# Kernel optimization log

Measured on AMD Instinct MI355X. Metric: run time of the kernel, lower is better.

## Reference

```python
import jax, jax.numpy as jnp
import numpy as np

N_NOTE = 14  # undefined global in original; must equal output_size for one-hot feedback


def setup_inputs() -> dict:
    key = jax.random.key(0)
    ks = jax.random.split(key, 9)
    B, T, H, O = 256, 512, 2048, 14
    s_i = 1.0 / np.sqrt(14)
    s_h = 1.0 / np.sqrt(H)
    return {
        "encoder_outputs": jax.random.normal(ks[0], (B, 1, H), jnp.float32),
        "encoder_hidden": jax.random.normal(ks[1], (1, B, H), jnp.float32),
        "target_tensor": jax.random.uniform(ks[2], (B, T, O), jnp.float32),
        "W_ih": jax.random.normal(ks[3], (3 * H, 14), jnp.float32) * s_i,
        "W_hh": jax.random.normal(ks[4], (3 * H, H), jnp.float32) * s_h,
        "b_ih": jax.random.normal(ks[5], (3 * H,), jnp.float32) * s_h,
        "b_hh": jax.random.normal(ks[6], (3 * H,), jnp.float32) * s_h,
        "W_out": jax.random.normal(ks[7], (O, H), jnp.float32) * s_h,
        "b_out": jax.random.normal(ks[8], (O,), jnp.float32) * s_h,
    }


def _decode(encoder_hidden, target_tensor, W_ih, W_hh, b_ih, b_hh, W_out, b_out):
    B, T, O = target_tensor.shape
    H = W_hh.shape[1]

    def step(carry, _):
        h, x = carry  # h: [B,H], x: [B,14]
        xr = jax.nn.relu(x)
        gi = xr @ W_ih.T + b_ih            # [B,3H]
        gh = h @ W_hh.T + b_hh             # [B,3H]
        r = jax.nn.sigmoid(gi[:, :H] + gh[:, :H])
        z = jax.nn.sigmoid(gi[:, H:2 * H] + gh[:, H:2 * H])
        n = jnp.tanh(gi[:, 2 * H:] + r * gh[:, 2 * H:])
        h_new = (1.0 - z) * n + z * h
        logits = h_new @ W_out.T + b_out   # [B,O]
        # feedback: one-hot of argmax; the Python `break` in the original zeros
        # every batch element at-or-after the first hit of n_note-1
        topi = jnp.argmax(logits, axis=-1)                     # [B]
        hit = (topi == N_NOTE - 1).astype(jnp.int32)
        alive = (jnp.cumsum(hit) == 0).astype(logits.dtype)    # inclusive cumsum
        x_next = jax.nn.one_hot(topi, O, dtype=logits.dtype) * alive[:, None]
        return (h_new, x_next), logits

    h0 = encoder_hidden[0]          # [B,H]
    x0 = target_tensor[:, 0]        # [B,14] first-step input
    (h_final, _), logits = jax.lax.scan(step, (h0, x0), None, length=T)
    logits = jnp.transpose(logits, (1, 0, 2))  # [B,T,O]
    log_probs = jax.nn.log_softmax(logits, axis=-1)
    return log_probs, h_final[None]  # ([B,T,O], [1,B,H])


def reference(encoder_outputs, encoder_hidden, target_tensor, W_ih, W_hh, b_ih, b_hh, W_out, b_out):
    # encoder_outputs is accepted but unused, matching the original forward
    return _decode(encoder_hidden, target_tensor, W_ih, W_hh, b_ih, b_hh, W_out, b_out)
```

## Files before the change

kernel.cpp:

```cpp
#include <hip/hip_runtime.h>
#include <math.h>

typedef float f4 __attribute__((ext_vector_type(4)));
typedef _Float16 f16x8 __attribute__((ext_vector_type(8)));
typedef int i4 __attribute__((ext_vector_type(4)));

#define Hdim 2048
#define Bdim 256
#define Tdim 512
#define Odim 14
#define G3   6144


__global__ void prep_gtable(const float* __restrict__ b_ih,
                            const float* __restrict__ W_ih,
                            float* __restrict__ Gt) {
    int idx = blockIdx.x * 256 + threadIdx.x;
    if (idx >= 15 * G3) return;
    int c = idx / G3, row = idx % G3;
    float v = b_ih[row];
    if (c < Odim) v += W_ih[row * Odim + c];
    Gt[idx] = v;
}

__global__ void prep_gi0(const float* __restrict__ b_ih,
                         const float* __restrict__ W_ih,
                         const float* __restrict__ target,
                         float* __restrict__ gi0) {
    int idx = blockIdx.x * 256 + threadIdx.x;
    int b = idx / G3, row = idx % G3;
    const float* x0 = target + (size_t)b * (Tdim * Odim);
    float s = b_ih[row];
    #pragma unroll
    for (int c = 0; c < Odim; ++c)
        s = fmaf(fmaxf(x0[c], 0.f), W_ih[row * Odim + c], s);
    gi0[idx] = s;
}

__global__ void prep_Bpack(const float* __restrict__ W,
                           _Float16* __restrict__ Bh, _Float16* __restrict__ Bl) {
    int idx = blockIdx.x * 256 + threadIdx.x;
    int n = idx >> 8, kc = idx & 255;
    const float* src = W + (size_t)n * Hdim + kc * 8;
    int kb = kc >> 2, q = kc & 3;
    int lane = (n & 15) + 16 * q;
    int nt = n >> 4;
    f16x8 vh, vl;
    #pragma unroll
    for (int j = 0; j < 8; ++j) {
        float w = src[j];
        _Float16 h = (_Float16)w;
        vh[j] = h;
        vl[j] = (_Float16)(w - (float)h);
    }
    size_t off = (((size_t)nt * 64 + kb) * 64 + lane) * 8;
    *(f16x8*)(Bh + off) = vh;
    *(f16x8*)(Bl + off) = vl;
}

__global__ void prep_A0(const float* __restrict__ h0,
                        _Float16* __restrict__ Ah, _Float16* __restrict__ Al) {
    int idx = blockIdx.x * 256 + threadIdx.x;
    int m = idx >> 8, kc = idx & 255;
    const float* src = h0 + (size_t)m * Hdim + kc * 8;
    int kb = kc >> 2, q = kc & 3;
    int lane = (m & 15) + 16 * q;
    int mt = m >> 4;
    f16x8 vh, vl;
    #pragma unroll
    for (int j = 0; j < 8; ++j) {
        float w = src[j];
        _Float16 h = (_Float16)w;
        vh[j] = h;
        vl[j] = (_Float16)(w - (float)h);
    }
    size_t off = (((size_t)mt * 64 + kb) * 64 + lane) * 8;
    *(f16x8*)(Ah + off) = vh;
    *(f16x8*)(Al + off) = vl;
}

__global__ __launch_bounds__(512, 1)
void gemm_step(const _Float16* __restrict__ Ah, const _Float16* __restrict__ Al,
               const _Float16* __restrict__ Bh, const _Float16* __restrict__ Bl,
               float* __restrict__ Cpart) {
    __shared__ __align__(16) _Float16 sB[2][24576];

    const int tid = threadIdx.x;
    const int wave = tid >> 6, lane = tid & 63;
    const int nt0 = blockIdx.x * 6;
    const int kb0 = blockIdx.y * 16;

    f4 acc[2][6];
    #pragma unroll
    for (int mf = 0; mf < 2; ++mf)
        #pragma unroll
        for (int nf = 0; nf < 6; ++nf) acc[mf][nf] = (f4)0.f;

    i4 rh[3], rl[3];

    #pragma unroll
    for (int i = 0; i < 3; ++i) {
        int e = i * 512 + tid, blk = e >> 6, l = e & 63;
        int ntl = blk >> 2, kbl = blk & 3;
        size_t off = (((size_t)(nt0 + ntl) * 64) + kb0 + kbl) * 512 + l * 8;
        rh[i] = *(const i4*)(Bh + off);
        rl[i] = *(const i4*)(Bl + off);
    }
    #pragma unroll
    for (int i = 0; i < 3; ++i) {
        ((i4*)sB[0])[i * 512 + tid] = rh[i];
        ((i4*)sB[0])[1536 + i * 512 + tid] = rl[i];
    }
    __syncthreads();

    for (int c = 0; c < 4; ++c) {
        const int buf = c & 1;
        if (c < 3) {
            #pragma unroll
            for (int i = 0; i < 3; ++i) {
                int e = i * 512 + tid, blk = e >> 6, l = e & 63;
                int ntl = blk >> 2, kbl = blk & 3;
                size_t off = (((size_t)(nt0 + ntl) * 64) + kb0 + (c + 1) * 4 + kbl) * 512 + l * 8;
                rh[i] = *(const i4*)(Bh + off);
                rl[i] = *(const i4*)(Bl + off);
            }
        }
        #pragma unroll
        for (int kbl = 0; kbl < 4; ++kbl) {
            const int kb = kb0 + c * 4 + kbl;
            f16x8 a_h[2], a_l[2], b_h[6], b_l[6];
            #pragma unroll
            for (int mf = 0; mf < 2; ++mf) {
                size_t off = (((size_t)(wave * 2 + mf) * 64 + kb) * 64 + lane) * 8;
                a_h[mf] = *(const f16x8*)(Ah + off);
                a_l[mf] = *(const f16x8*)(Al + off);
            }
            #pragma unroll
            for (int nf = 0; nf < 6; ++nf) {
                int base = (nf * 4 + kbl) * 512 + lane * 8;
                b_h[nf] = *(const f16x8*)(&sB[buf][base]);
                b_l[nf] = *(const f16x8*)(&sB[buf][12288 + base]);
            }
            #pragma unroll
            for (int mf = 0; mf < 2; ++mf)
                #pragma unroll
                for (int nf = 0; nf < 6; ++nf) {
                    acc[mf][nf] = __builtin_amdgcn_mfma_f32_16x16x32_f16(
                        a_h[mf], b_h[nf], acc[mf][nf], 0, 0, 0);
                    acc[mf][nf] = __builtin_amdgcn_mfma_f32_16x16x32_f16(
                        a_h[mf], b_l[nf], acc[mf][nf], 0, 0, 0);
                    acc[mf][nf] = __builtin_amdgcn_mfma_f32_16x16x32_f16(
                        a_l[mf], b_h[nf], acc[mf][nf], 0, 0, 0);
                }
        }
        if (c < 3) {
            __syncthreads();
            #pragma unroll
            for (int i = 0; i < 3; ++i) {
                ((i4*)sB[buf ^ 1])[i * 512 + tid] = rh[i];
                ((i4*)sB[buf ^ 1])[1536 + i * 512 + tid] = rl[i];
            }
            __syncthreads();
        }
    }

    const size_t base = (size_t)blockIdx.y * 256 * G3;
    #pragma unroll
    for (int mf = 0; mf < 2; ++mf) {
        int mrow = wave * 32 + mf * 16 + (lane >> 4) * 4;
        #pragma unroll
        for (int nf = 0; nf < 6; ++nf) {
            int n = (nt0 + nf) * 16 + (lane & 15);
            #pragma unroll
            for (int q = 0; q < 4; ++q)
                Cpart[base + (size_t)(mrow + q) * G3 + n] = acc[mf][nf][q];
        }
    }
}

__global__ __launch_bounds__(256)
void fused_out(const float* __restrict__ hprev, float* __restrict__ hnew,
               const float* __restrict__ Cpart, const float* __restrict__ Gt,
               const float* __restrict__ gi0, const float* __restrict__ b_hh,
               const float* __restrict__ W_out, const float* __restrict__ b_out,
               _Float16* __restrict__ Ah, _Float16* __restrict__ Al,
               const int* __restrict__ topi_in, int* __restrict__ topi_out,
               float* __restrict__ lp, float* __restrict__ hfin, int t) {
    const int b = blockIdx.x;
    const int tid = threadIdx.x;
    __shared__ __align__(16) float sh[Hdim];
    __shared__ float sl[16];
    __shared__ int s_sel;
    __shared__ unsigned long long s_m[4];

    if (t > 0) {
        int tp = topi_in[tid];
        unsigned long long m = __ballot(tp == (Odim - 1));
        if ((tid & 63) == 0) s_m[tid >> 6] = m;
        __syncthreads();
        if (tid == 0) {
            int bw = b >> 6, bl = b & 63;
            unsigned long long le =
                s_m[bw] & ((bl == 63) ? ~0ULL : ((1ULL << (bl + 1)) - 1ULL));
            bool dead = (le != 0ULL);
            for (int w = 0; w < bw; ++w) dead = dead || (s_m[w] != 0ULL);
            s_sel = dead ? Odim : topi_in[b];
        }
        __syncthreads();
    }
    const float* gp = (t == 0) ? (gi0 + (size_t)b * G3)
                               : (Gt + (size_t)s_sel * G3);

    const int j0 = tid * 8;
    float hn[8];
    {
        float gsum[3][8];
        #pragma unroll
        for (int g = 0; g < 3; ++g) {
            f4 s0 = *(const f4*)(b_hh + g * Hdim + j0);
            f4 s1 = *(const f4*)(b_hh + g * Hdim + j0 + 4);
            #pragma unroll
            for (int c = 0; c < 4; ++c) { gsum[g][c] = s0[c]; gsum[g][4 + c] = s1[c]; }
            #pragma unroll
            for (int ks = 0; ks < 4; ++ks) {
                const float* cp = Cpart + ((size_t)ks * Bdim + b) * G3 + g * Hdim + j0;
                f4 p0 = *(const f4*)cp;
                f4 p1 = *(const f4*)(cp + 4);
                #pragma unroll
                for (int c = 0; c < 4; ++c) { gsum[g][c] += p0[c]; gsum[g][4 + c] += p1[c]; }
            }
        }
        f4 hp0 = *(const f4*)(hprev + (size_t)b * Hdim + j0);
        f4 hp1 = *(const f4*)(hprev + (size_t)b * Hdim + j0 + 4);
        f4 gr0 = *(const f4*)(gp + j0),            gr1 = *(const f4*)(gp + j0 + 4);
        f4 gz0 = *(const f4*)(gp + Hdim + j0),     gz1 = *(const f4*)(gp + Hdim + j0 + 4);
        f4 gn0 = *(const f4*)(gp + 2 * Hdim + j0), gn1 = *(const f4*)(gp + 2 * Hdim + j0 + 4);
        #pragma unroll
        for (int c = 0; c < 8; ++c) {
            float gi_r = (c < 4) ? gr0[c] : gr1[c - 4];
            float gi_z = (c < 4) ? gz0[c] : gz1[c - 4];
            float gi_n = (c < 4) ? gn0[c] : gn1[c - 4];
            float hp   = (c < 4) ? hp0[c] : hp1[c - 4];
            float rr = 1.f / (1.f + expf(-(gi_r + gsum[0][c])));
            float zz = 1.f / (1.f + expf(-(gi_z + gsum[1][c])));
            float nn = tanhf(fmaf(rr, gsum[2][c], gi_n));
            hn[c] = (1.f - zz) * nn + zz * hp;
        }
    }
    f4 o0, o1;
    #pragma unroll
    for (int c = 0; c < 4; ++c) { o0[c] = hn[c]; o1[c] = hn[4 + c]; }
    *(f4*)(hnew + (size_t)b * Hdim + j0) = o0;
    *(f4*)(hnew + (size_t)b * Hdim + j0 + 4) = o1;
    {
        f16x8 vh, vl;
        #pragma unroll
        for (int c = 0; c < 8; ++c) {
            _Float16 hh = (_Float16)hn[c];
            vh[c] = hh;
            vl[c] = (_Float16)(hn[c] - (float)hh);
        }
        int kb = tid >> 2, q = tid & 3;
        int lane = (b & 15) + 16 * q, mt = b >> 4;
        size_t off = (((size_t)mt * 64 + kb) * 64 + lane) * 8;
        *(f16x8*)(Ah + off) = vh;
        *(f16x8*)(Al + off) = vl;
    }
    *(f4*)(sh + j0) = o0;
    *(f4*)(sh + j0 + 4) = o1;
    __syncthreads();

    const int w = tid >> 6, l = tid & 63;
    for (int o = w; o < Odim; o += 4) {
        const float* wo = W_out + (size_t)o * Hdim;
        float s = 0.f;
        #pragma unroll
        for (int i = 0; i < 32; ++i)
            s = fmaf(sh[l + 64 * i], wo[l + 64 * i], s);
        #pragma unroll
        for (int off = 32; off >= 1; off >>= 1)
            s += __shfl_down(s, off);
        if (l == 0) sl[o] = s + b_out[o];
    }
    __syncthreads();
    if (tid == 0) {
        float m = sl[0]; int bi = 0;
        #pragma unroll
        for (int o = 1; o < Odim; ++o)
            if (sl[o] > m) { m = sl[o]; bi = o; }
        float ssum = 0.f;
        #pragma unroll
        for (int o = 0; o < Odim; ++o) ssum += expf(sl[o] - m);
        topi_out[b] = bi;
        sl[14] = m + logf(ssum);
    }
    __syncthreads();
    if (tid < Odim)
        lp[(size_t)b * (Tdim * Odim) + (size_t)t * Odim + tid] = sl[tid] - sl[14];
    if (hfin) {
        *(f4*)(hfin + (size_t)b * Hdim + j0) = o0;
        *(f4*)(hfin + (size_t)b * Hdim + j0 + 4) = o1;
    }
}

extern "C" void kernel_launch(void* const* d_in, const int* in_sizes, int n_in,
                              void* d_out, int out_size, void* d_ws, size_t ws_size,
                              hipStream_t stream) {
    const float* enc_hidden = (const float*)d_in[1];
    const float* target     = (const float*)d_in[2];
    const float* W_ih       = (const float*)d_in[3];
    const float* W_hh       = (const float*)d_in[4];
    const float* b_ih       = (const float*)d_in[5];
    const float* b_hh       = (const float*)d_in[6];
    const float* W_out      = (const float*)d_in[7];
    const float* b_out      = (const float*)d_in[8];

    float* out  = (float*)d_out;
    float* lp   = out;
    float* hfin = out + (size_t)Bdim * Tdim * Odim;

    float* ws    = (float*)d_ws;
    float* hb0   = ws;
    float* hb1   = hb0 + 524288;
    float* Gt    = hb1 + 524288;
    float* gi0   = Gt + 15 * G3;
    float* Cpart = gi0 + (size_t)Bdim * G3;
    _Float16* Ah = (_Float16*)(Cpart + 4 * (size_t)Bdim * G3);
    _Float16* Al = Ah + (size_t)Bdim * Hdim;
    _Float16* Bh = Al + (size_t)Bdim * Hdim;
    _Float16* Bl = Bh + (size_t)G3 * Hdim;
    int* topibuf = (int*)(Bl + (size_t)G3 * Hdim);

    prep_gtable<<<(15 * G3 + 255) / 256, 256, 0, stream>>>(b_ih, W_ih, Gt);
    prep_gi0<<<(Bdim * G3) / 256, 256, 0, stream>>>(b_ih, W_ih, target, gi0);
    prep_Bpack<<<(G3 * 256) / 256, 256, 0, stream>>>(W_hh, Bh, Bl);
    prep_A0<<<(Bdim * 256) / 256, 256, 0, stream>>>(enc_hidden, Ah, Al);

    for (int t = 0; t < Tdim; ++t) {
        float* hnew = (t & 1) ? hb1 : hb0;
        const float* hprev = (t == 0) ? enc_hidden : ((t & 1) ? hb0 : hb1);
        int* tin  = topibuf + ((t + 1) & 1) * 256;
        int* tout = topibuf + (t & 1) * 256;
        gemm_step<<<dim3(64, 4), 512, 0, stream>>>(Ah, Al, Bh, Bl, Cpart);
        fused_out<<<256, 256, 0, stream>>>(hprev, hnew, Cpart, Gt, gi0, b_hh,
                                           W_out, b_out, Ah, Al, tin, tout, lp,
                                           (t == Tdim - 1) ? hfin : nullptr, t);
    }
}
```

Baseline: 19.93 ms.

## Retile recurrent GEMM to 3 N-tiles with 2-way K split, widen fused_out

```diff
diff --git a/kernel.cpp b/kernel.cpp
--- a/kernel.cpp
+++ b/kernel.cpp
@@ -3,6 +3,7 @@
 
 typedef float f4 __attribute__((ext_vector_type(4)));
 typedef _Float16 f16x8 __attribute__((ext_vector_type(8)));
+typedef _Float16 f16x4 __attribute__((ext_vector_type(4)));
 typedef int i4 __attribute__((ext_vector_type(4)));
 
 #define Hdim 2048
@@ -79,7 +80,7 @@
     *(f16x8*)(Al + off) = vl;
 }
 
-__global__ __launch_bounds__(512, 1)
+__global__ __launch_bounds__(512, 2)
 void gemm_step(const _Float16* __restrict__ Ah, const _Float16* __restrict__ Al,
                const _Float16* __restrict__ Bh, const _Float16* __restrict__ Bl,
                float* __restrict__ Cpart) {
@@ -87,21 +88,21 @@
 
     const int tid = threadIdx.x;
     const int wave = tid >> 6, lane = tid & 63;
-    const int nt0 = blockIdx.x * 6;
-    const int kb0 = blockIdx.y * 16;
-
-    f4 acc[2][6];
+    const int nt0 = blockIdx.x * 3;
+    const int kb0 = blockIdx.y * 32;
+
+    f4 acc[2][3];
     #pragma unroll
     for (int mf = 0; mf < 2; ++mf)
         #pragma unroll
-        for (int nf = 0; nf < 6; ++nf) acc[mf][nf] = (f4)0.f;
+        for (int nf = 0; nf < 3; ++nf) acc[mf][nf] = (f4)0.f;
 
     i4 rh[3], rl[3];
 
     #pragma unroll
     for (int i = 0; i < 3; ++i) {
         int e = i * 512 + tid, blk = e >> 6, l = e & 63;
-        int ntl = blk >> 2, kbl = blk & 3;
+        int ntl = blk >> 3, kbl = blk & 7;
         size_t off = (((size_t)(nt0 + ntl) * 64) + kb0 + kbl) * 512 + l * 8;
         rh[i] = *(const i4*)(Bh + off);
         rl[i] = *(const i4*)(Bl + off);
@@ -119,16 +120,16 @@
             #pragma unroll
             for (int i = 0; i < 3; ++i) {
                 int e = i * 512 + tid, blk = e >> 6, l = e & 63;
-                int ntl = blk >> 2, kbl = blk & 3;
-                size_t off = (((size_t)(nt0 + ntl) * 64) + kb0 + (c + 1) * 4 + kbl) * 512 + l * 8;
+                int ntl = blk >> 3, kbl = blk & 7;
+                size_t off = (((size_t)(nt0 + ntl) * 64) + kb0 + (c + 1) * 8 + kbl) * 512 + l * 8;
                 rh[i] = *(const i4*)(Bh + off);
                 rl[i] = *(const i4*)(Bl + off);
             }
         }
         #pragma unroll
-        for (int kbl = 0; kbl < 4; ++kbl) {
-            const int kb = kb0 + c * 4 + kbl;
-            f16x8 a_h[2], a_l[2], b_h[6], b_l[6];
+        for (int kbl = 0; kbl < 8; ++kbl) {
+            const int kb = kb0 + c * 8 + kbl;
+            f16x8 a_h[2], a_l[2], b_h[3], b_l[3];
             #pragma unroll
             for (int mf = 0; mf < 2; ++mf) {
                 size_t off = (((size_t)(wave * 2 + mf) * 64 + kb) * 64 + lane) * 8;
@@ -136,15 +137,15 @@
                 a_l[mf] = *(const f16x8*)(Al + off);
             }
             #pragma unroll
-            for (int nf = 0; nf < 6; ++nf) {
-                int base = (nf * 4 + kbl) * 512 + lane * 8;
+            for (int nf = 0; nf < 3; ++nf) {
+                int base = ((nf * 8 + kbl) * 64 + lane) * 8;
                 b_h[nf] = *(const f16x8*)(&sB[buf][base]);
                 b_l[nf] = *(const f16x8*)(&sB[buf][12288 + base]);
             }
             #pragma unroll
             for (int mf = 0; mf < 2; ++mf)
                 #pragma unroll
-                for (int nf = 0; nf < 6; ++nf) {
+                for (int nf = 0; nf < 3; ++nf) {
                     acc[mf][nf] = __builtin_amdgcn_mfma_f32_16x16x32_f16(
                         a_h[mf], b_h[nf], acc[mf][nf], 0, 0, 0);
                     acc[mf][nf] = __builtin_amdgcn_mfma_f32_16x16x32_f16(
@@ -164,12 +165,12 @@
         }
     }
 
-    const size_t base = (size_t)blockIdx.y * 256 * G3;
+    const size_t base = (size_t)blockIdx.y * Bdim * G3;
     #pragma unroll
     for (int mf = 0; mf < 2; ++mf) {
         int mrow = wave * 32 + mf * 16 + (lane >> 4) * 4;
         #pragma unroll
-        for (int nf = 0; nf < 6; ++nf) {
+        for (int nf = 0; nf < 3; ++nf) {
             int n = (nt0 + nf) * 16 + (lane & 15);
             #pragma unroll
             for (int q = 0; q < 4; ++q)
@@ -178,7 +179,7 @@
     }
 }
 
-__global__ __launch_bounds__(256)
+__global__ __launch_bounds__(512)
 void fused_out(const float* __restrict__ hprev, float* __restrict__ hnew,
                const float* __restrict__ Cpart, const float* __restrict__ Gt,
                const float* __restrict__ gi0, const float* __restrict__ b_hh,
@@ -194,9 +195,11 @@
     __shared__ unsigned long long s_m[4];
 
     if (t > 0) {
-        int tp = topi_in[tid];
-        unsigned long long m = __ballot(tp == (Odim - 1));
-        if ((tid & 63) == 0) s_m[tid >> 6] = m;
+        if (tid < 256) {
+            int tp = topi_in[tid];
+            unsigned long long m = __ballot(tp == (Odim - 1));
+            if ((tid & 63) == 0) s_m[tid >> 6] = m;
+        }
         __syncthreads();
         if (tid == 0) {
             int bw = b >> 6, bl = b & 63;
@@ -211,67 +214,54 @@
     const float* gp = (t == 0) ? (gi0 + (size_t)b * G3)
                                : (Gt + (size_t)s_sel * G3);
 
-    const int j0 = tid * 8;
-    float hn[8];
+    const int j0 = tid * 4;
+    float hn[4];
     {
-        float gsum[3][8];
+        float gsum[3][4];
         #pragma unroll
         for (int g = 0; g < 3; ++g) {
-            f4 s0 = *(const f4*)(b_hh + g * Hdim + j0);
-            f4 s1 = *(const f4*)(b_hh + g * Hdim + j0 + 4);
-            #pragma unroll
-            for (int c = 0; c < 4; ++c) { gsum[g][c] = s0[c]; gsum[g][4 + c] = s1[c]; }
-            #pragma unroll
-            for (int ks = 0; ks < 4; ++ks) {
-                const float* cp = Cpart + ((size_t)ks * Bdim + b) * G3 + g * Hdim + j0;
-                f4 p0 = *(const f4*)cp;
-                f4 p1 = *(const f4*)(cp + 4);
-                #pragma unroll
-                for (int c = 0; c < 4; ++c) { gsum[g][c] += p0[c]; gsum[g][4 + c] += p1[c]; }
-            }
-        }
-        f4 hp0 = *(const f4*)(hprev + (size_t)b * Hdim + j0);
-        f4 hp1 = *(const f4*)(hprev + (size_t)b * Hdim + j0 + 4);
-        f4 gr0 = *(const f4*)(gp + j0),            gr1 = *(const f4*)(gp + j0 + 4);
-        f4 gz0 = *(const f4*)(gp + Hdim + j0),     gz1 = *(const f4*)(gp + Hdim + j0 + 4);
-        f4 gn0 = *(const f4*)(gp + 2 * Hdim + j0), gn1 = *(const f4*)(gp + 2 * Hdim + j0 + 4);
-        #pragma unroll
-        for (int c = 0; c < 8; ++c) {
-            float gi_r = (c < 4) ? gr0[c] : gr1[c - 4];
-            float gi_z = (c < 4) ? gz0[c] : gz1[c - 4];
-            float gi_n = (c < 4) ? gn0[c] : gn1[c - 4];
-            float hp   = (c < 4) ? hp0[c] : hp1[c - 4];
-            float rr = 1.f / (1.f + expf(-(gi_r + gsum[0][c])));
-            float zz = 1.f / (1.f + expf(-(gi_z + gsum[1][c])));
-            float nn = tanhf(fmaf(rr, gsum[2][c], gi_n));
-            hn[c] = (1.f - zz) * nn + zz * hp;
-        }
-    }
-    f4 o0, o1;
-    #pragma unroll
-    for (int c = 0; c < 4; ++c) { o0[c] = hn[c]; o1[c] = hn[4 + c]; }
+            f4 s = *(const f4*)(b_hh + g * Hdim + j0);
+            #pragma unroll
+            for (int ks = 0; ks < 2; ++ks)
+                s += *(const f4*)(Cpart + ((size_t)ks * Bdim + b) * G3 + g * Hdim + j0);
+            #pragma unroll
+            for (int c = 0; c < 4; ++c) gsum[g][c] = s[c];
+        }
+        f4 hp = *(const f4*)(hprev + (size_t)b * Hdim + j0);
+        f4 gr = *(const f4*)(gp + j0);
+        f4 gz = *(const f4*)(gp + Hdim + j0);
+        f4 gn = *(const f4*)(gp + 2 * Hdim + j0);
+        #pragma unroll
+        for (int c = 0; c < 4; ++c) {
+            float rr = 1.f / (1.f + expf(-(gr[c] + gsum[0][c])));
+            float zz = 1.f / (1.f + expf(-(gz[c] + gsum[1][c])));
+            float nn = tanhf(fmaf(rr, gsum[2][c], gn[c]));
+            hn[c] = (1.f - zz) * nn + zz * hp[c];
+        }
+    }
+    f4 o0;
+    #pragma unroll
+    for (int c = 0; c < 4; ++c) o0[c] = hn[c];
     *(f4*)(hnew + (size_t)b * Hdim + j0) = o0;
-    *(f4*)(hnew + (size_t)b * Hdim + j0 + 4) = o1;
     {
-        f16x8 vh, vl;
-        #pragma unroll
-        for (int c = 0; c < 8; ++c) {
+        f16x4 vh, vl;
+        #pragma unroll
+        for (int c = 0; c < 4; ++c) {
             _Float16 hh = (_Float16)hn[c];
             vh[c] = hh;
             vl[c] = (_Float16)(hn[c] - (float)hh);
         }
-        int kb = tid >> 2, q = tid & 3;
+        int kb = j0 >> 5, q = (j0 >> 3) & 3, e0 = j0 & 7;
         int lane = (b & 15) + 16 * q, mt = b >> 4;
-        size_t off = (((size_t)mt * 64 + kb) * 64 + lane) * 8;
-        *(f16x8*)(Ah + off) = vh;
-        *(f16x8*)(Al + off) = vl;
+        size_t off = (((size_t)mt * 64 + kb) * 64 + lane) * 8 + e0;
+        *(f16x4*)(Ah + off) = vh;
+        *(f16x4*)(Al + off) = vl;
     }
     *(f4*)(sh + j0) = o0;
-    *(f4*)(sh + j0 + 4) = o1;
     __syncthreads();
 
     const int w = tid >> 6, l = tid & 63;
-    for (int o = w; o < Odim; o += 4) {
+    for (int o = w; o < Odim; o += 8) {
         const float* wo = W_out + (size_t)o * Hdim;
         float s = 0.f;
         #pragma unroll
@@ -297,10 +287,8 @@
     __syncthreads();
     if (tid < Odim)
         lp[(size_t)b * (Tdim * Odim) + (size_t)t * Odim + tid] = sl[tid] - sl[14];
-    if (hfin) {
+    if (hfin)
         *(f4*)(hfin + (size_t)b * Hdim + j0) = o0;
-        *(f4*)(hfin + (size_t)b * Hdim + j0 + 4) = o1;
-    }
 }
 
 extern "C" void kernel_launch(void* const* d_in, const int* in_sizes, int n_in,
@@ -341,8 +329,8 @@
         const float* hprev = (t == 0) ? enc_hidden : ((t & 1) ? hb0 : hb1);
         int* tin  = topibuf + ((t + 1) & 1) * 256;
         int* tout = topibuf + (t & 1) * 256;
-        gemm_step<<<dim3(64, 4), 512, 0, stream>>>(Ah, Al, Bh, Bl, Cpart);
-        fused_out<<<256, 256, 0, stream>>>(hprev, hnew, Cpart, Gt, gi0, b_hh,
+        gemm_step<<<dim3(128, 2), 512, 0, stream>>>(Ah, Al, Bh, Bl, Cpart);
+        fused_out<<<256, 512, 0, stream>>>(hprev, hnew, Cpart, Gt, gi0, b_hh,
                                            W_out, b_out, Ah, Al, tin, tout, lp,
                                            (t == Tdim - 1) ? hfin : nullptr, t);
     }
```

After: 19.32 ms. 3.1% less time.
